# Kernel optimization log

Measured on AMD Instinct MI355X. Metric: run time of the kernel, lower is better.

## Reference

```python
import jax, jax.numpy as jnp
import numpy as np

D = 2048
H = 16
DH = D // H  # 128
B = 512
EPS = 1e-5


def _layernorm(x, g, b):
    m = jnp.mean(x, axis=-1, keepdims=True)
    v = jnp.mean((x - m) ** 2, axis=-1, keepdims=True)
    return (x - m) * jax.lax.rsqrt(v + EPS) * g + b


def setup_inputs() -> dict:
    key = jax.random.key(0)
    ks = jax.random.split(key, 16)
    s_in = 1.0 / np.sqrt(D)
    s_ff = 1.0 / np.sqrt(4 * D)
    return {
        "x": jax.random.normal(ks[0], (B, D), jnp.float32),
        # per-head q/k/v projections, stacked over heads: [H, D, DH]
        "Wq": jax.random.uniform(ks[1], (H, D, DH), jnp.float32, -s_in, s_in),
        "bq": jax.random.uniform(ks[2], (H, DH), jnp.float32, -s_in, s_in),
        "Wk": jax.random.uniform(ks[3], (H, D, DH), jnp.float32, -s_in, s_in),
        "bk": jax.random.uniform(ks[4], (H, DH), jnp.float32, -s_in, s_in),
        "Wv": jax.random.uniform(ks[5], (H, D, DH), jnp.float32, -s_in, s_in),
        "bv": jax.random.uniform(ks[6], (H, DH), jnp.float32, -s_in, s_in),
        "Wo": jax.random.uniform(ks[7], (D, D), jnp.float32, -s_in, s_in),
        "bo": jax.random.uniform(ks[8], (D,), jnp.float32, -s_in, s_in),
        "W1": jax.random.uniform(ks[9], (D, 4 * D), jnp.float32, -s_in, s_in),
        "b1": jax.random.uniform(ks[10], (4 * D,), jnp.float32, -s_in, s_in),
        "W2": jax.random.uniform(ks[11], (4 * D, D), jnp.float32, -s_ff, s_ff),
        "b2": jax.random.uniform(ks[12], (D,), jnp.float32, -s_ff, s_ff),
        "g1": jnp.ones((D,), jnp.float32),
        "be1": jnp.zeros((D,), jnp.float32),
        "g2": jnp.ones((D,), jnp.float32),
        "be2": jnp.zeros((D,), jnp.float32),
    }


def reference(x, Wq, bq, Wk, bk, Wv, bv, Wo, bo, W1, b1, W2, b2, g1, be1, g2, be2):
    # --- pre-norm attention branch ---
    h = _layernorm(x, g1, be1)                       # [B, D]
    q = jnp.einsum('bd,hde->bhe', h, Wq) + bq        # [B, H, DH]
    k = jnp.einsum('bd,hde->bhe', h, Wk) + bk
    v = jnp.einsum('bd,hde->bhe', h, Wv) + bv
    # outer-product 'attention' per sample: [B, H, DH, DH]
    attn = q[..., :, None] * k[..., None, :] / jnp.sqrt(jnp.float32(DH))
    attn = jax.nn.softmax(attn, axis=-1)
    o = jnp.einsum('bhij,bhj->bhi', attn, v)         # [B, H, DH]
    o = o.reshape(x.shape[0], H * DH)                # concat over heads
    x = x + o @ Wo + bo
    # --- pre-norm FFN branch ---
    h2 = _layernorm(x, g2, be2)
    x = x + jax.nn.relu(h2 @ W1 + b1) @ W2 + b2
    return x
```

## Files before the change

### kernel.cpp

```cpp
#include <hip/hip_runtime.h>
#include <hip/hip_bf16.h>
#include <math.h>


#define DDIM 2048
#define HHEADS 16
#define DHEAD 128
#define BROWS 512
#define LN_EPS 1e-5f

typedef __bf16 bf16x8_t __attribute__((ext_vector_type(8)));
typedef float f32x4_t __attribute__((ext_vector_type(4)));

#define GLD16(gptr, lptr)                                                     \
    __builtin_amdgcn_global_load_lds(                                         \
        (const __attribute__((address_space(1))) void*)(gptr),                \
        (__attribute__((address_space(3))) void*)(lptr), 16, 0, 0)

__global__ __launch_bounds__(256) void ln_kernel(const float* __restrict__ x,
                                                 const float* __restrict__ g,
                                                 const float* __restrict__ b,
                                                 __bf16* __restrict__ out) {
    const int row = blockIdx.x;
    const int tid = threadIdx.x;
    const float4* x4 = (const float4*)(x + (size_t)row * DDIM);
    float4 a = x4[2 * tid];
    float4 c = x4[2 * tid + 1];
    float s  = a.x + a.y + a.z + a.w + c.x + c.y + c.z + c.w;
    float s2 = a.x*a.x + a.y*a.y + a.z*a.z + a.w*a.w
             + c.x*c.x + c.y*c.y + c.z*c.z + c.w*c.w;
    #pragma unroll
    for (int off = 32; off > 0; off >>= 1) {
        s  += __shfl_down(s, off);
        s2 += __shfl_down(s2, off);
    }
    __shared__ float ps[4], ps2[4];
    __shared__ float mean_s, rstd_s;
    const int lane = tid & 63, w = tid >> 6;
    if (lane == 0) { ps[w] = s; ps2[w] = s2; }
    __syncthreads();
    if (tid == 0) {
        float S  = ps[0] + ps[1] + ps[2] + ps[3];
        float S2 = ps2[0] + ps2[1] + ps2[2] + ps2[3];
        float m  = S * (1.0f / DDIM);
        float var = S2 * (1.0f / DDIM) - m * m;
        mean_s = m;
        rstd_s = rsqrtf(var + LN_EPS);
    }
    __syncthreads();
    const float m = mean_s, r = rstd_s;
    const float4* g4 = (const float4*)g;
    const float4* b4 = (const float4*)b;
    float4 ga = g4[2 * tid], gb = g4[2 * tid + 1];
    float4 ba = b4[2 * tid], bb = b4[2 * tid + 1];
    bf16x8_t o;
    o[0] = (__bf16)((a.x - m) * r * ga.x + ba.x);
    o[1] = (__bf16)((a.y - m) * r * ga.y + ba.y);
    o[2] = (__bf16)((a.z - m) * r * ga.z + ba.z);
    o[3] = (__bf16)((a.w - m) * r * ga.w + ba.w);
    o[4] = (__bf16)((c.x - m) * r * gb.x + bb.x);
    o[5] = (__bf16)((c.y - m) * r * gb.y + bb.y);
    o[6] = (__bf16)((c.z - m) * r * gb.z + bb.z);
    o[7] = (__bf16)((c.w - m) * r * gb.w + bb.w);
    *(bf16x8_t*)(out + (size_t)row * DDIM + tid * 8) = o;
}

__global__ __launch_bounds__(256) void transpose_kernel(
    const float* __restrict__ src, __bf16* __restrict__ dst, int R, int C) {
    __shared__ float tile[32][33];
    const size_t bofs = (size_t)blockIdx.z * R * C;
    src += bofs;
    dst += bofs;
    const int c0 = blockIdx.x * 32, r0 = blockIdx.y * 32;
    const int tx = threadIdx.x & 31, ty = threadIdx.x >> 5;
    #pragma unroll
    for (int i = 0; i < 32; i += 8)
        tile[ty + i][tx] = src[(size_t)(r0 + ty + i) * C + c0 + tx];
    __syncthreads();
    #pragma unroll
    for (int i = 0; i < 32; i += 8)
        dst[(size_t)(c0 + ty + i) * R + r0 + tx] = (__bf16)tile[tx][ty + i];
}

__global__ __launch_bounds__(256) void fuse_bias_kernel(
    const float* __restrict__ bq, const float* __restrict__ bk,
    const float* __restrict__ bv, float* __restrict__ fb) {
    const int i = blockIdx.x * 256 + threadIdx.x;
    float v;
    if (i < 2048) v = bq[i];
    else if (i < 4096) v = bk[i - 2048];
    else v = bv[i - 4096];
    fb[i] = v;
}

template <int TM, int TN, int OUT_BF16, int RELU, int RES>
__global__ __launch_bounds__(256) void gemm_bt(
    const __bf16* __restrict__ A, int K,
    const __bf16* __restrict__ Bt,
    const float* __restrict__ bias,
    const float* __restrict__ Res,
    void* __restrict__ Cout, int N) {
    constexpr int DEPTH = 4;
    constexpr int STG = (TM + TN) * 32;
    __shared__ __align__(16) __bf16 smem[DEPTH * STG];

    const int tid = threadIdx.x;
    const int w = tid >> 6, lane = tid & 63;
    const int m0 = blockIdx.y * TM, n0 = blockIdx.x * TN;

    constexpr int NA = TM / 16;
    constexpr int NT = (TM + TN) / 16;
    constexpr int NI = NT / 4;

    const int sub_r = lane >> 2;
    const int sub_k = (lane & 3) * 8;

    const __bf16* srcs[NI];
    int toff[NI];
    #pragma unroll
    for (int i = 0; i < NI; i++) {
        const int t = w + 4 * i;
        toff[i] = t * 512;
        if (t < NA)
            srcs[i] = A + (size_t)(m0 + t * 16 + sub_r) * K + sub_k;
        else
            srcs[i] = Bt + (size_t)(n0 + (t - NA) * 16 + sub_r) * K + sub_k;
    }

    constexpr int MI = TM / 32;
    constexpr int NJ = TN / 32;
    const int wm = (w >> 1) * (TM / 2), wn = (w & 1) * (TN / 2);
    const int fm = lane & 15, quad = lane >> 4;

    f32x4_t acc[MI][NJ] = {};

    const int NK = K / 32;

    #pragma unroll
    for (int d = 0; d < DEPTH; d++)
        #pragma unroll
        for (int i = 0; i < NI; i++)
            GLD16(srcs[i] + d * 32, smem + d * STG + toff[i]);

    for (int ks = 0; ks < NK; ks++) {
        const __bf16* st = smem + (ks & (DEPTH - 1)) * STG;
        asm volatile("s_waitcnt vmcnt(%0)\n\ts_barrier"
                     :: "i"((DEPTH - 1) * NI) : "memory");

        bf16x8_t a[MI], b[NJ];
        #pragma unroll
        for (int i = 0; i < MI; i++)
            a[i] = *(const bf16x8_t*)&st[(wm + i * 16 + fm) * 32 + quad * 8];
        #pragma unroll
        for (int j = 0; j < NJ; j++)
            b[j] = *(const bf16x8_t*)&st[TM * 32 + (wn + j * 16 + fm) * 32 + quad * 8];
        #pragma unroll
        for (int i = 0; i < MI; i++)
            #pragma unroll
            for (int j = 0; j < NJ; j++)
                acc[i][j] = __builtin_amdgcn_mfma_f32_16x16x32_bf16(
                    a[i], b[j], acc[i][j], 0, 0, 0);

        asm volatile("s_waitcnt lgkmcnt(0)\n\ts_barrier" ::: "memory");
        if (ks + DEPTH < NK) {
            __bf16* dst = smem + (ks & (DEPTH - 1)) * STG;
            #pragma unroll
            for (int i = 0; i < NI; i++)
                GLD16(srcs[i] + (ks + DEPTH) * 32, dst + toff[i]);
        }
    }

    #pragma unroll
    for (int i = 0; i < MI; i++) {
        #pragma unroll
        for (int j = 0; j < NJ; j++) {
            const int col = n0 + wn + j * 16 + fm;
            const float bcol = bias[col];
            #pragma unroll
            for (int r = 0; r < 4; r++) {
                const int row = m0 + wm + i * 16 + quad * 4 + r;
                float val = acc[i][j][r] + bcol;
                if (RES) val += Res[(size_t)row * N + col];
                if (RELU) val = fmaxf(val, 0.0f);
                if (OUT_BF16)
                    ((__bf16*)Cout)[(size_t)row * N + col] = (__bf16)val;
                else
                    ((float*)Cout)[(size_t)row * N + col] = val;
            }
        }
    }
}

__global__ __launch_bounds__(128) void attn_kernel(
    const __bf16* __restrict__ qkv, __bf16* __restrict__ o) {
    const int bh = blockIdx.x;
    const int b = bh >> 4, h = bh & 15;
    const size_t base = (size_t)b * (3 * DDIM) + h * DHEAD;
    const int tid = threadIdx.x;
    __shared__ float ks[DHEAD], vs[DHEAD];
    ks[tid] = (float)qkv[base + DDIM + tid];
    vs[tid] = (float)qkv[base + 2 * DDIM + tid];
    __syncthreads();
    const float a = (float)qkv[base + tid] * 0.08838834764831845f;
    float den = 0.0f, num = 0.0f;
    #pragma unroll 8
    for (int j = 0; j < DHEAD; j++) {
        float e = __expf(a * ks[j]);
        den += e;
        num += e * vs[j];
    }
    o[(size_t)b * DDIM + h * DHEAD + tid] = (__bf16)(num / den);
}

extern "C" void kernel_launch(void* const* d_in, const int* in_sizes, int n_in,
                              void* d_out, int out_size, void* d_ws, size_t ws_size,
                              hipStream_t stream) {
    const float* x   = (const float*)d_in[0];
    const float* Wq  = (const float*)d_in[1];
    const float* bq  = (const float*)d_in[2];
    const float* Wk  = (const float*)d_in[3];
    const float* bk  = (const float*)d_in[4];
    const float* Wv  = (const float*)d_in[5];
    const float* bv  = (const float*)d_in[6];
    const float* Wo  = (const float*)d_in[7];
    const float* bo  = (const float*)d_in[8];
    const float* W1  = (const float*)d_in[9];
    const float* b1  = (const float*)d_in[10];
    const float* W2  = (const float*)d_in[11];
    const float* b2  = (const float*)d_in[12];
    const float* g1  = (const float*)d_in[13];
    const float* be1 = (const float*)d_in[14];
    const float* g2  = (const float*)d_in[15];
    const float* be2 = (const float*)d_in[16];
    float* out = (float*)d_out;

    char* base = (char*)d_ws;
    float*  fb     = (float*)(base + 0);
    __bf16* bt_qkv = (__bf16*)(base + 32768);
    char*   slotA  = base + 32768 + 25165824;
    char*   slotB  = slotA + 33554432;
    __bf16* h   = (__bf16*)(slotB + 0);
    __bf16* qkv = (__bf16*)(slotB + 2097152);
    __bf16* ob  = (__bf16*)(slotB + 8388608);
    float*  x1  = (float*)((char*)bt_qkv + 0);
    __bf16* h2  = (__bf16*)((char*)bt_qkv + 4194304);
    __bf16* t   = (__bf16*)((char*)bt_qkv + 6291456);
    __bf16* Wot = (__bf16*)slotA;
    __bf16* W1t = (__bf16*)slotB;
    __bf16* W2t = (__bf16*)slotA;

    fuse_bias_kernel<<<24, 256, 0, stream>>>(bq, bk, bv, fb);

    transpose_kernel<<<dim3(4, 64, 16), 256, 0, stream>>>(Wq, bt_qkv, DDIM, DHEAD);
    transpose_kernel<<<dim3(4, 64, 16), 256, 0, stream>>>(Wk, bt_qkv + 2048 * 2048, DDIM, DHEAD);
    transpose_kernel<<<dim3(4, 64, 16), 256, 0, stream>>>(Wv, bt_qkv + 2 * 2048 * 2048, DDIM, DHEAD);
    transpose_kernel<<<dim3(64, 64, 1), 256, 0, stream>>>(Wo, Wot, DDIM, DDIM);

    ln_kernel<<<BROWS, 256, 0, stream>>>(x, g1, be1, h);

    gemm_bt<64, 128, 1, 0, 0><<<dim3(48, 8), 256, 0, stream>>>(
        h, DDIM, bt_qkv, fb, nullptr, qkv, 3 * DDIM);

    attn_kernel<<<BROWS * HHEADS, 128, 0, stream>>>(qkv, ob);

    gemm_bt<64, 64, 0, 0, 1><<<dim3(32, 8), 256, 0, stream>>>(
        ob, DDIM, Wot, bo, x, x1, DDIM);

    transpose_kernel<<<dim3(256, 64, 1), 256, 0, stream>>>(W1, W1t, DDIM, 4 * DDIM);
    transpose_kernel<<<dim3(64, 256, 1), 256, 0, stream>>>(W2, W2t, 4 * DDIM, DDIM);

    ln_kernel<<<BROWS, 256, 0, stream>>>(x1, g2, be2, h2);

    gemm_bt<64, 128, 1, 1, 0><<<dim3(64, 8), 256, 0, stream>>>(
        h2, DDIM, W1t, b1, nullptr, t, 4 * DDIM);

    gemm_bt<64, 64, 0, 0, 1><<<dim3(32, 8), 256, 0, stream>>>(
        t, 4 * DDIM, W2t, b2, x1, out, DDIM);
}
```

Baseline: 404.3 us.

## Use 64x64 tiles everywhere and split-K the Wo and W2 GEMMs

The GEMM kernel is fixed to a 64x64 tile with a simpler one-load-per-wave staging layout. The output-projection and W2 GEMMs become split-K (2 and 4 slices) writing fp32 partials, and a new elementwise kernel sums the partials with bias and residual. The aim is more blocks to fill the GPU's compute units for the narrow N=2048 GEMMs. The cost is extra partial-buffer traffic and an added launch. Workspace buffers are reorganised and the W1 transpose is moved earlier; the main loop now always issues prefetch loads, which are redundant on the last iterations.

Result: slower. 483.3 us (+19.5%).

```diff
diff --git a/kernel.cpp b/kernel.cpp
--- a/kernel.cpp
+++ b/kernel.cpp
@@ -93,102 +93,106 @@
     fb[i] = v;
 }
 
-template <int TM, int TN, int OUT_BF16, int RELU, int RES>
+template <int OUT_BF16, int RELU, int BIAS>
 __global__ __launch_bounds__(256) void gemm_bt(
-    const __bf16* __restrict__ A, int K,
-    const __bf16* __restrict__ Bt,
+    const __bf16* __restrict__ A, int lda,
+    const __bf16* __restrict__ Bt, int ldb,
+    int nk,
+    int kslice,
     const float* __restrict__ bias,
-    const float* __restrict__ Res,
-    void* __restrict__ Cout, int N) {
+    void* __restrict__ Cout, int N, long long zstride) {
     constexpr int DEPTH = 4;
-    constexpr int STG = (TM + TN) * 32;
+    constexpr int STG = 4096;
     __shared__ __align__(16) __bf16 smem[DEPTH * STG];
 
     const int tid = threadIdx.x;
     const int w = tid >> 6, lane = tid & 63;
-    const int m0 = blockIdx.y * TM, n0 = blockIdx.x * TN;
-
-    constexpr int NA = TM / 16;
-    constexpr int NT = (TM + TN) / 16;
-    constexpr int NI = NT / 4;
-
-    const int sub_r = lane >> 2;
-    const int sub_k = (lane & 3) * 8;
-
-    const __bf16* srcs[NI];
-    int toff[NI];
-    #pragma unroll
-    for (int i = 0; i < NI; i++) {
-        const int t = w + 4 * i;
-        toff[i] = t * 512;
-        if (t < NA)
-            srcs[i] = A + (size_t)(m0 + t * 16 + sub_r) * K + sub_k;
-        else
-            srcs[i] = Bt + (size_t)(n0 + (t - NA) * 16 + sub_r) * K + sub_k;
-    }
-
-    constexpr int MI = TM / 32;
-    constexpr int NJ = TN / 32;
-    const int wm = (w >> 1) * (TM / 2), wn = (w & 1) * (TN / 2);
+    const int m0 = blockIdx.y * 64, n0 = blockIdx.x * 64;
+    const int z = blockIdx.z;
+
+    const __bf16* Az = A + (size_t)z * kslice;
+    const __bf16* Bz = Bt + (size_t)z * kslice;
+
+    const int sub_r = lane & 15;
+    const int sub_k = (lane >> 4) * 8;
+    const __bf16* srcA = Az + (size_t)(m0 + w * 16 + sub_r) * lda + sub_k;
+    const __bf16* srcB = Bz + (size_t)(n0 + w * 16 + sub_r) * ldb + sub_k;
+    const int offA = w * 512;
+    const int offB = 2048 + w * 512;
+
+    const int wm = (w >> 1) * 32, wn = (w & 1) * 32;
     const int fm = lane & 15, quad = lane >> 4;
-
-    f32x4_t acc[MI][NJ] = {};
-
-    const int NK = K / 32;
-
-    #pragma unroll
-    for (int d = 0; d < DEPTH; d++)
-        #pragma unroll
-        for (int i = 0; i < NI; i++)
-            GLD16(srcs[i] + d * 32, smem + d * STG + toff[i]);
-
-    for (int ks = 0; ks < NK; ks++) {
+    const int cmA = (w >> 1) * 2;
+    const int cnB = (w & 1) * 2;
+
+    f32x4_t acc[2][2] = {};
+
+    #pragma unroll
+    for (int d = 0; d < DEPTH; d++) {
+        GLD16(srcA + d * 32, smem + d * STG + offA);
+        GLD16(srcB + d * 32, smem + d * STG + offB);
+    }
+
+    for (int ks = 0; ks < nk; ks++) {
         const __bf16* st = smem + (ks & (DEPTH - 1)) * STG;
-        asm volatile("s_waitcnt vmcnt(%0)\n\ts_barrier"
-                     :: "i"((DEPTH - 1) * NI) : "memory");
-
-        bf16x8_t a[MI], b[NJ];
-        #pragma unroll
-        for (int i = 0; i < MI; i++)
-            a[i] = *(const bf16x8_t*)&st[(wm + i * 16 + fm) * 32 + quad * 8];
-        #pragma unroll
-        for (int j = 0; j < NJ; j++)
-            b[j] = *(const bf16x8_t*)&st[TM * 32 + (wn + j * 16 + fm) * 32 + quad * 8];
-        #pragma unroll
-        for (int i = 0; i < MI; i++)
+        asm volatile("s_waitcnt vmcnt(6)\n\ts_barrier" ::: "memory");
+
+        bf16x8_t a[2], b[2];
+        #pragma unroll
+        for (int i = 0; i < 2; i++)
+            a[i] = *(const bf16x8_t*)&st[(cmA + i) * 512 + lane * 8];
+        #pragma unroll
+        for (int j = 0; j < 2; j++)
+            b[j] = *(const bf16x8_t*)&st[2048 + (cnB + j) * 512 + lane * 8];
+        #pragma unroll
+        for (int i = 0; i < 2; i++)
             #pragma unroll
-            for (int j = 0; j < NJ; j++)
+            for (int j = 0; j < 2; j++)
                 acc[i][j] = __builtin_amdgcn_mfma_f32_16x16x32_bf16(
                     a[i], b[j], acc[i][j], 0, 0, 0);
 
         asm volatile("s_waitcnt lgkmcnt(0)\n\ts_barrier" ::: "memory");
-        if (ks + DEPTH < NK) {
-            __bf16* dst = smem + (ks & (DEPTH - 1)) * STG;
-            #pragma unroll
-            for (int i = 0; i < NI; i++)
-                GLD16(srcs[i] + (ks + DEPTH) * 32, dst + toff[i]);
-        }
-    }
-
-    #pragma unroll
-    for (int i = 0; i < MI; i++) {
-        #pragma unroll
-        for (int j = 0; j < NJ; j++) {
+        const int kk = (ks + DEPTH < nk) ? (ks + DEPTH) : 0;
+        __bf16* dst = smem + (ks & (DEPTH - 1)) * STG;
+        GLD16(srcA + kk * 32, dst + offA);
+        GLD16(srcB + kk * 32, dst + offB);
+    }
+
+    #pragma unroll
+    for (int i = 0; i < 2; i++) {
+        #pragma unroll
+        for (int j = 0; j < 2; j++) {
             const int col = n0 + wn + j * 16 + fm;
-            const float bcol = bias[col];
+            const float bcol = BIAS ? bias[col] : 0.0f;
             #pragma unroll
             for (int r = 0; r < 4; r++) {
                 const int row = m0 + wm + i * 16 + quad * 4 + r;
                 float val = acc[i][j][r] + bcol;
-                if (RES) val += Res[(size_t)row * N + col];
                 if (RELU) val = fmaxf(val, 0.0f);
                 if (OUT_BF16)
                     ((__bf16*)Cout)[(size_t)row * N + col] = (__bf16)val;
                 else
-                    ((float*)Cout)[(size_t)row * N + col] = val;
+                    ((float*)Cout)[z * zstride + (size_t)row * N + col] = val;
             }
         }
     }
+}
+
+template <int SPLITS>
+__global__ __launch_bounds__(256) void fuse_kernel(
+    const float* __restrict__ base_in, const float* __restrict__ p,
+    const float* __restrict__ bias, float* __restrict__ out) {
+    const size_t i4 = (size_t)blockIdx.x * 256 + threadIdx.x;
+    const int col4 = i4 & (DDIM / 4 - 1);
+    float4 v = ((const float4*)base_in)[i4];
+    float4 bb = ((const float4*)bias)[col4];
+    v.x += bb.x; v.y += bb.y; v.z += bb.z; v.w += bb.w;
+    #pragma unroll
+    for (int s = 0; s < SPLITS; s++) {
+        float4 q = ((const float4*)p)[s * (BROWS * DDIM / 4) + i4];
+        v.x += q.x; v.y += q.y; v.z += q.z; v.w += q.w;
+    }
+    ((float4*)out)[i4] = v;
 }
 
 __global__ __launch_bounds__(128) void attn_kernel(
@@ -235,19 +239,24 @@
     float* out = (float*)d_out;
 
     char* base = (char*)d_ws;
-    float*  fb     = (float*)(base + 0);
-    __bf16* bt_qkv = (__bf16*)(base + 32768);
-    char*   slotA  = base + 32768 + 25165824;
-    char*   slotB  = slotA + 33554432;
-    __bf16* h   = (__bf16*)(slotB + 0);
-    __bf16* qkv = (__bf16*)(slotB + 2097152);
-    __bf16* ob  = (__bf16*)(slotB + 8388608);
-    float*  x1  = (float*)((char*)bt_qkv + 0);
-    __bf16* h2  = (__bf16*)((char*)bt_qkv + 4194304);
-    __bf16* t   = (__bf16*)((char*)bt_qkv + 6291456);
-    __bf16* Wot = (__bf16*)slotA;
-    __bf16* W1t = (__bf16*)slotB;
-    __bf16* W2t = (__bf16*)slotA;
+    float*  fb     = (float*)(base);
+    char*   R1     = base + 32768;
+    char*   R2     = R1 + 33554432;
+    char*   R3     = R2 + 33554432;
+    __bf16* bt_qkv = (__bf16*)R1;
+    __bf16* Wot    = (__bf16*)(R1 + 25165824);
+    __bf16* W2t    = (__bf16*)R1;
+    __bf16* W1t    = (__bf16*)R2;
+    float*  w2_p   = (float*)R2;
+    float*  x1     = (float*)R3;
+    char*   hq     = R3 + 4194304;
+    __bf16* h      = (__bf16*)hq;
+    __bf16* qkv    = (__bf16*)(hq + 2097152);
+    float*  wo_p   = (float*)hq;
+    __bf16* t      = (__bf16*)hq;
+    char*   obslot = R3 + 12582912;
+    __bf16* ob     = (__bf16*)obslot;
+    __bf16* h2     = (__bf16*)obslot;
 
     fuse_bias_kernel<<<24, 256, 0, stream>>>(bq, bk, bv, fb);
 
@@ -255,25 +264,29 @@
     transpose_kernel<<<dim3(4, 64, 16), 256, 0, stream>>>(Wk, bt_qkv + 2048 * 2048, DDIM, DHEAD);
     transpose_kernel<<<dim3(4, 64, 16), 256, 0, stream>>>(Wv, bt_qkv + 2 * 2048 * 2048, DDIM, DHEAD);
     transpose_kernel<<<dim3(64, 64, 1), 256, 0, stream>>>(Wo, Wot, DDIM, DDIM);
+    transpose_kernel<<<dim3(256, 64, 1), 256, 0, stream>>>(W1, W1t, DDIM, 4 * DDIM);
 
     ln_kernel<<<BROWS, 256, 0, stream>>>(x, g1, be1, h);
 
-    gemm_bt<64, 128, 1, 0, 0><<<dim3(48, 8), 256, 0, stream>>>(
-        h, DDIM, bt_qkv, fb, nullptr, qkv, 3 * DDIM);
+    gemm_bt<1, 0, 1><<<dim3(96, 8), 256, 0, stream>>>(
+        h, DDIM, bt_qkv, DDIM, 64, 0, fb, qkv, 3 * DDIM, 0);
 
     attn_kernel<<<BROWS * HHEADS, 128, 0, stream>>>(qkv, ob);
 
-    gemm_bt<64, 64, 0, 0, 1><<<dim3(32, 8), 256, 0, stream>>>(
-        ob, DDIM, Wot, bo, x, x1, DDIM);
-
-    transpose_kernel<<<dim3(256, 64, 1), 256, 0, stream>>>(W1, W1t, DDIM, 4 * DDIM);
+    gemm_bt<0, 0, 0><<<dim3(32, 8, 2), 256, 0, stream>>>(
+        ob, DDIM, Wot, DDIM, 32, 1024, nullptr, wo_p, DDIM,
+        (long long)BROWS * DDIM);
+    fuse_kernel<2><<<1024, 256, 0, stream>>>(x, wo_p, bo, x1);
+
+    ln_kernel<<<BROWS, 256, 0, stream>>>(x1, g2, be2, h2);
+
+    gemm_bt<1, 1, 1><<<dim3(128, 8), 256, 0, stream>>>(
+        h2, DDIM, W1t, DDIM, 64, 0, b1, t, 4 * DDIM, 0);
+
     transpose_kernel<<<dim3(64, 256, 1), 256, 0, stream>>>(W2, W2t, 4 * DDIM, DDIM);
 
-    ln_kernel<<<BROWS, 256, 0, stream>>>(x1, g2, be2, h2);
-
-    gemm_bt<64, 128, 1, 1, 0><<<dim3(64, 8), 256, 0, stream>>>(
-        h2, DDIM, W1t, b1, nullptr, t, 4 * DDIM);
-
-    gemm_bt<64, 64, 0, 0, 1><<<dim3(32, 8), 256, 0, stream>>>(
-        t, 4 * DDIM, W2t, b2, x1, out, DDIM);
-}
+    gemm_bt<0, 0, 0><<<dim3(32, 8, 4), 256, 0, stream>>>(
+        t, 4 * DDIM, W2t, 4 * DDIM, 64, 2048, nullptr, w2_p, DDIM,
+        (long long)BROWS * DDIM);
+    fuse_kernel<4><<<1024, 256, 0, stream>>>(x1, w2_p, b2, out);
+}
```
